# Optimization experiments

Measured on AMD Instinct MI355X. Metric: run time of the kernel, lower is better.

The kernel has to match this reference:

```python
import jax, jax.numpy as jnp
import numpy as np

B, T, D_IN, NB = 8, 4096, 128, 32  # batch, frames, in_dim, n_basis
STRIDE = 2


def setup_inputs() -> dict:
    key = jax.random.key(0)
    kx, ke, kf = jax.random.split(key, 3)
    std = np.sqrt(2.0 / (D_IN + NB)).astype(np.float32)
    return {
        "X": jax.random.normal(kx, (B, T, D_IN), dtype=jnp.float32),
        "E": jax.random.normal(ke, (D_IN, NB), dtype=jnp.float32) * std,
        "F": jax.random.normal(kf, (D_IN, NB), dtype=jnp.float32) * std,
        "G": jnp.ones((1,), dtype=jnp.float32),
        "bx": jnp.zeros((NB,), dtype=jnp.float32),
        "by": jnp.zeros((NB,), dtype=jnp.float32),
    }


def reference(X, E, F, G, bx, by):
    # z1, z2: [B, T, NB]
    z1 = jnp.einsum("btd,dn->btn", X, E) + bx
    z2 = jnp.einsum("btd,dn->btn", X, F) + by
    # per-frame outer product -> [B, T, NB*NB], scaled by G
    z = G[0] * (z1[..., :, None] * z2[..., None, :]).reshape(B, T, NB * NB)
    # AveragePooling1D(pool_size=stride, strides=stride, padding='same');
    # T divisible by STRIDE so 'same' adds no padding.
    out_pool = z.reshape(B, T // STRIDE, STRIDE, NB * NB).mean(axis=2)
    return out_pool
```

## Files before the change

kernel.cpp:

```cpp
#include <hip/hip_runtime.h>


#define DIN 128
#define NB_ 32

constexpr int N2   = 64;
constexpr int FR   = 64;
constexpr int POOL = 32;
constexpr int SXS  = 132;
constexpr int SZS  = 68;
constexpr int NBLK = (8 * 4096) / FR;

__global__ __launch_bounds__(256) void trp_fused(
    const float* __restrict__ X, const float* __restrict__ E,
    const float* __restrict__ F, const float* __restrict__ G,
    const float* __restrict__ bx, const float* __restrict__ by,
    float* __restrict__ out)
{
    __shared__ __align__(16) float sw[DIN * N2];
    __shared__ __align__(16) float sxz[FR * SXS];

    const int tid = threadIdx.x;
    const int blk = blockIdx.x;

    #pragma unroll
    for (int it = 0; it < 8; ++it) {
        int v = tid + 256 * it;
        int d = v >> 4, c = v & 15;
        const float* src = (c < 8) ? (E + d * NB_ + c * 4)
                                   : (F + d * NB_ + (c - 8) * 4);
        float4 val = *(const float4*)src;
        *(float4*)&sw[d * N2 + c * 4] = val;
    }
    const float* xb = X + (size_t)blk * FR * DIN;
    #pragma unroll
    for (int it = 0; it < 8; ++it) {
        int v = tid + 256 * it;
        int f = v >> 5, dc = v & 31;
        float4 val = *(const float4*)(xb + f * DIN + dc * 4);
        *(float4*)&sxz[f * SXS + dc * 4] = val;
    }
    __syncthreads();

    const int n0 = (tid & 15) * 4;
    const int f0 = (tid >> 4) * 4;

    float acc[4][4];
    #pragma unroll
    for (int q = 0; q < 4; ++q)
        #pragma unroll
        for (int c = 0; c < 4; ++c) acc[q][c] = 0.f;

    #pragma unroll 2
    for (int dc = 0; dc < DIN / 4; ++dc) {
        const int d4 = dc * 4;
        float w[4][4];
        #pragma unroll
        for (int r = 0; r < 4; ++r)
            *(float4*)&w[r][0] = *(const float4*)&sw[(d4 + r) * N2 + n0];
        #pragma unroll
        for (int q = 0; q < 4; ++q) {
            float x[4];
            *(float4*)&x[0] = *(const float4*)&sxz[(f0 + q) * SXS + d4];
            #pragma unroll
            for (int r = 0; r < 4; ++r)
                #pragma unroll
                for (int c = 0; c < 4; ++c)
                    acc[q][c] = fmaf(x[r], w[r][c], acc[q][c]);
        }
    }

    float bias[4];
    if (n0 < NB_) *(float4*)bias = *(const float4*)(bx + n0);
    else          *(float4*)bias = *(const float4*)(by + (n0 - NB_));

    __syncthreads();
    #pragma unroll
    for (int q = 0; q < 4; ++q) {
        float4 z;
        z.x = acc[q][0] + bias[0];
        z.y = acc[q][1] + bias[1];
        z.z = acc[q][2] + bias[2];
        z.w = acc[q][3] + bias[3];
        *(float4*)&sxz[(f0 + q) * SZS + n0] = z;
    }
    __syncthreads();

    const float g2 = 0.5f * G[0];
    const int i = tid >> 3;
    const int j = (tid & 7) * 4;
    float4* outv = (float4*)out + (size_t)blk * (POOL * 256) + tid;
    #pragma unroll 4
    for (int p = 0; p < POOL; ++p) {
        const float* zr0 = &sxz[(2 * p) * SZS];
        const float* zr1 = &sxz[(2 * p + 1) * SZS];
        float a0 = zr0[i];
        float a1 = zr1[i];
        float4 v0 = *(const float4*)&zr0[NB_ + j];
        float4 v1 = *(const float4*)&zr1[NB_ + j];
        float4 r;
        r.x = g2 * fmaf(a0, v0.x, a1 * v1.x);
        r.y = g2 * fmaf(a0, v0.y, a1 * v1.y);
        r.z = g2 * fmaf(a0, v0.z, a1 * v1.z);
        r.w = g2 * fmaf(a0, v0.w, a1 * v1.w);
        outv[p * 256] = r;
    }
}

extern "C" void kernel_launch(void* const* d_in, const int* in_sizes, int n_in,
                              void* d_out, int out_size, void* d_ws, size_t ws_size,
                              hipStream_t stream) {
    const float* X  = (const float*)d_in[0];
    const float* E  = (const float*)d_in[1];
    const float* F  = (const float*)d_in[2];
    const float* G  = (const float*)d_in[3];
    const float* bx = (const float*)d_in[4];
    const float* by = (const float*)d_in[5];
    float* out = (float*)d_out;
    trp_fused<<<dim3(NBLK), dim3(256), 0, stream>>>(X, E, F, G, bx, by, out);
}
```

Before: 96.57 us.

## Halve block size, double per-thread frames, make waves own private frame slices

Blocks drop from 256 to 128 threads. Each thread now computes two 4x4 accumulator tiles (frames 32 apart), so each weight load from LDS is reused twice. Each wave writes its z rows into its own slice of shared memory, which removes one block barrier and lets the pooled outer-product stage read only rows written by the same wave. The weight LDS stride is padded to 68 to reduce bank conflicts, and the 0.5*G scale is folded into z1. In exchange, registers per thread roughly double and the global loads are split across fewer threads.

Result: slower. 112.4 us (+16.3%).

```diff
diff --git a/kernel.cpp b/kernel.cpp
--- a/kernel.cpp
+++ b/kernel.cpp
@@ -4,52 +4,53 @@
 #define DIN 128
 #define NB_ 32
 
-constexpr int N2   = 64;
 constexpr int FR   = 64;
-constexpr int POOL = 32;
 constexpr int SXS  = 132;
+constexpr int SWS  = 68;
 constexpr int SZS  = 68;
 constexpr int NBLK = (8 * 4096) / FR;
 
-__global__ __launch_bounds__(256) void trp_fused(
+__global__ __launch_bounds__(128) void trp_fused(
     const float* __restrict__ X, const float* __restrict__ E,
     const float* __restrict__ F, const float* __restrict__ G,
     const float* __restrict__ bx, const float* __restrict__ by,
     float* __restrict__ out)
 {
-    __shared__ __align__(16) float sw[DIN * N2];
+    __shared__ __align__(16) float sw[DIN * SWS];
     __shared__ __align__(16) float sxz[FR * SXS];
 
     const int tid = threadIdx.x;
     const int blk = blockIdx.x;
 
     #pragma unroll
-    for (int it = 0; it < 8; ++it) {
-        int v = tid + 256 * it;
+    for (int it = 0; it < 16; ++it) {
+        int v = tid + 128 * it;
         int d = v >> 4, c = v & 15;
         const float* src = (c < 8) ? (E + d * NB_ + c * 4)
                                    : (F + d * NB_ + (c - 8) * 4);
-        float4 val = *(const float4*)src;
-        *(float4*)&sw[d * N2 + c * 4] = val;
+        *(float4*)&sw[d * SWS + c * 4] = *(const float4*)src;
     }
     const float* xb = X + (size_t)blk * FR * DIN;
     #pragma unroll
-    for (int it = 0; it < 8; ++it) {
-        int v = tid + 256 * it;
+    for (int it = 0; it < 16; ++it) {
+        int v = tid + 128 * it;
         int f = v >> 5, dc = v & 31;
-        float4 val = *(const float4*)(xb + f * DIN + dc * 4);
-        *(float4*)&sxz[f * SXS + dc * 4] = val;
+        *(float4*)&sxz[f * SXS + dc * 4] = *(const float4*)(xb + f * DIN + dc * 4);
     }
     __syncthreads();
 
-    const int n0 = (tid & 15) * 4;
-    const int f0 = (tid >> 4) * 4;
+    const int wave = tid >> 6;
+    const int n0   = (tid & 15) * 4;
+    const int fg   = (tid >> 4) & 3;
+    const int fA   = wave * 16 + fg * 4;
 
-    float acc[4][4];
+    float acc[2][4][4];
     #pragma unroll
-    for (int q = 0; q < 4; ++q)
+    for (int cl = 0; cl < 2; ++cl)
         #pragma unroll
-        for (int c = 0; c < 4; ++c) acc[q][c] = 0.f;
+        for (int q = 0; q < 4; ++q)
+            #pragma unroll
+            for (int c = 0; c < 4; ++c) acc[cl][q][c] = 0.f;
 
     #pragma unroll 2
     for (int dc = 0; dc < DIN / 4; ++dc) {
@@ -57,53 +58,71 @@
         float w[4][4];
         #pragma unroll
         for (int r = 0; r < 4; ++r)
-            *(float4*)&w[r][0] = *(const float4*)&sw[(d4 + r) * N2 + n0];
+            *(float4*)&w[r][0] = *(const float4*)&sw[(d4 + r) * SWS + n0];
         #pragma unroll
-        for (int q = 0; q < 4; ++q) {
-            float x[4];
-            *(float4*)&x[0] = *(const float4*)&sxz[(f0 + q) * SXS + d4];
+        for (int cl = 0; cl < 2; ++cl) {
             #pragma unroll
-            for (int r = 0; r < 4; ++r)
+            for (int q = 0; q < 4; ++q) {
+                float x[4];
+                *(float4*)&x[0] = *(const float4*)&sxz[(fA + cl * 32 + q) * SXS + d4];
                 #pragma unroll
-                for (int c = 0; c < 4; ++c)
-                    acc[q][c] = fmaf(x[r], w[r][c], acc[q][c]);
+                for (int r = 0; r < 4; ++r)
+                    #pragma unroll
+                    for (int c = 0; c < 4; ++c)
+                        acc[cl][q][c] = fmaf(x[r], w[r][c], acc[cl][q][c]);
+            }
         }
     }
 
-    float bias[4];
-    if (n0 < NB_) *(float4*)bias = *(const float4*)(bx + n0);
-    else          *(float4*)bias = *(const float4*)(by + (n0 - NB_));
+    float bias[4], scale;
+    if (n0 < NB_) { *(float4*)bias = *(const float4*)(bx + n0);       scale = 0.5f * G[0]; }
+    else          { *(float4*)bias = *(const float4*)(by + n0 - NB_); scale = 1.0f; }
 
-    __syncthreads();
     #pragma unroll
-    for (int q = 0; q < 4; ++q) {
-        float4 z;
-        z.x = acc[q][0] + bias[0];
-        z.y = acc[q][1] + bias[1];
-        z.z = acc[q][2] + bias[2];
-        z.w = acc[q][3] + bias[3];
-        *(float4*)&sxz[(f0 + q) * SZS + n0] = z;
+    for (int cl = 0; cl < 2; ++cl) {
+        const int zb = (cl * 32 + wave * 16) * SXS;
+        #pragma unroll
+        for (int q = 0; q < 4; ++q) {
+            float4 z;
+            z.x = (acc[cl][q][0] + bias[0]) * scale;
+            z.y = (acc[cl][q][1] + bias[1]) * scale;
+            z.z = (acc[cl][q][2] + bias[2]) * scale;
+            z.w = (acc[cl][q][3] + bias[3]) * scale;
+            *(float4*)&sxz[zb + (fg * 4 + q) * SZS + n0] = z;
+        }
     }
     __syncthreads();
 
-    const float g2 = 0.5f * G[0];
-    const int i = tid >> 3;
-    const int j = (tid & 7) * 4;
-    float4* outv = (float4*)out + (size_t)blk * (POOL * 256) + tid;
-    #pragma unroll 4
-    for (int p = 0; p < POOL; ++p) {
-        const float* zr0 = &sxz[(2 * p) * SZS];
-        const float* zr1 = &sxz[(2 * p + 1) * SZS];
-        float a0 = zr0[i];
-        float a1 = zr1[i];
-        float4 v0 = *(const float4*)&zr0[NB_ + j];
-        float4 v1 = *(const float4*)&zr1[NB_ + j];
-        float4 r;
-        r.x = g2 * fmaf(a0, v0.x, a1 * v1.x);
-        r.y = g2 * fmaf(a0, v0.y, a1 * v1.y);
-        r.z = g2 * fmaf(a0, v0.z, a1 * v1.z);
-        r.w = g2 * fmaf(a0, v0.w, a1 * v1.w);
-        outv[p * 256] = r;
+    const int lane = tid & 63;
+    const int j4 = lane & 7;
+    const int i0 = lane >> 3;
+    float4* out4 = (float4*)out;
+    const int pooledBase = blk * 32;
+
+    #pragma unroll
+    for (int cl = 0; cl < 2; ++cl) {
+        const int zb = (cl * 32 + wave * 16) * SXS;
+        const int pfBase = pooledBase + cl * 16 + wave * 8;
+        #pragma unroll 2
+        for (int pp = 0; pp < 8; ++pp) {
+            const float* zr0 = &sxz[zb + (2 * pp) * SZS];
+            const float* zr1 = zr0 + SZS;
+            float4 v0 = *(const float4*)&zr0[NB_ + 4 * j4];
+            float4 v1 = *(const float4*)&zr1[NB_ + 4 * j4];
+            float4* ob = out4 + (size_t)(pfBase + pp) * 256 + lane;
+            #pragma unroll
+            for (int t = 0; t < 4; ++t) {
+                const int i = i0 + 8 * t;
+                float a0 = zr0[i];
+                float a1 = zr1[i];
+                float4 r;
+                r.x = fmaf(a0, v0.x, a1 * v1.x);
+                r.y = fmaf(a0, v0.y, a1 * v1.y);
+                r.z = fmaf(a0, v0.z, a1 * v1.z);
+                r.w = fmaf(a0, v0.w, a1 * v1.w);
+                ob[64 * t] = r;
+            }
+        }
     }
 }
 
@@ -116,6 +135,6 @@
     const float* G  = (const float*)d_in[3];
     const float* bx = (const float*)d_in[4];
     const float* by = (const float*)d_in[5];
-    float* out = (float*)d_out;
-    trp_fused<<<dim3(NBLK), dim3(256), 0, stream>>>(X, E, F, G, bx, by, out);
+    float* outp = (float*)d_out;
+    trp_fused<<<dim3(NBLK), dim3(128), 0, stream>>>(X, E, F, G, bx, by, outp);
 }
```
